# Kernel tuning notes

Hardware: AMD Instinct MI355X
Metric: run time of the kernel (lower is better)

The kernel has to match this reference:

```python
import jax, jax.numpy as jnp
import numpy as np

B, L = 32, 4096
OBS_DIM, ACT_DIM = 32, 8
D_MODEL, D_STATE, N_LAYERS = 64, 16, 2
EXPAND, D_CONV = 2, 4
D_INNER = EXPAND * D_MODEL          # 128
DT_RANK = -(-D_MODEL // 16)         # ceil(64/16) = 4


def _layer_norm(x, w, b, eps=1e-5):
    m = x.mean(-1, keepdims=True)
    v = ((x - m) ** 2).mean(-1, keepdims=True)
    return (x - m) * jax.lax.rsqrt(v + eps) * w + b


def _mamba_block(x, in_proj_W, conv_w, conv_b, x_proj_W, dt_proj_W, dt_proj_b, A_log, D, out_proj_W):
    # x: (B, L, d_model) -> (B, L, d_model)
    xz = jnp.einsum('bld,ed->ble', x, in_proj_W)              # (B, L, 2*d_inner)
    u, z = jnp.split(xz, 2, axis=-1)
    # causal depthwise conv over time (groups = d_inner)
    uc = jax.lax.conv_general_dilated(u.swapaxes(1, 2), conv_w, (1,), [(D_CONV - 1, 0)],
                                      feature_group_count=D_INNER)
    u = jax.nn.silu((uc + conv_b[None, :, None]).swapaxes(1, 2))  # (B, L, d_inner)
    proj = jnp.einsum('bld,ed->ble', u, x_proj_W)             # (B, L, dt_rank + 2*d_state)
    dt = jax.nn.softplus(jnp.einsum('blr,dr->bld', proj[..., :DT_RANK], dt_proj_W) + dt_proj_b)
    Bm = proj[..., DT_RANK:DT_RANK + D_STATE]                 # (B, L, d_state)
    Cm = proj[..., DT_RANK + D_STATE:]                        # (B, L, d_state)
    A = -jnp.exp(A_log)                                       # (d_inner, d_state)

    def step(h, inp):
        u_t, dt_t, B_t, C_t = inp                              # (B,d_inner),(B,d_inner),(B,d_state),(B,d_state)
        h = h * jnp.exp(dt_t[..., None] * A) + (dt_t * u_t)[..., None] * B_t[:, None, :]
        return h, jnp.einsum('bds,bs->bd', h, C_t)

    h0 = jnp.zeros((x.shape[0], D_INNER, D_STATE), x.dtype)
    _, ys = jax.lax.scan(step, h0, (u.swapaxes(0, 1), dt.swapaxes(0, 1),
                                    Bm.swapaxes(0, 1), Cm.swapaxes(0, 1)))
    y = ys.swapaxes(0, 1) + u * D                              # skip term D*u
    y = y * jax.nn.silu(z)                                     # gated output
    return jnp.einsum('bld,od->blo', y, out_proj_W)


def setup_inputs() -> dict:
    key = jax.random.key(0)
    ks = jax.random.split(key, 10)
    s = 0.05
    return {
        'obs': jax.random.normal(ks[0], (B, L, OBS_DIM), jnp.float32),
        'obs_mean': jnp.zeros((OBS_DIM,), jnp.float32),
        'obs_scale': jnp.ones((OBS_DIM,), jnp.float32),
        'ln_in_w': jnp.ones((OBS_DIM,), jnp.float32),
        'ln_in_b': jnp.zeros((OBS_DIM,), jnp.float32),
        'W_in': jax.random.normal(ks[1], (D_MODEL, OBS_DIM), jnp.float32) * s,
        'b_in': jnp.zeros((D_MODEL,), jnp.float32),
        'norm_w': jnp.ones((N_LAYERS, D_MODEL), jnp.float32),
        'norm_b': jnp.zeros((N_LAYERS, D_MODEL), jnp.float32),
        'in_proj_W': jax.random.normal(ks[2], (N_LAYERS, 2 * D_INNER, D_MODEL), jnp.float32) * s,
        'conv_w': jax.random.normal(ks[3], (N_LAYERS, D_INNER, 1, D_CONV), jnp.float32) * s,
        'conv_b': jnp.zeros((N_LAYERS, D_INNER), jnp.float32),
        'x_proj_W': jax.random.normal(ks[4], (N_LAYERS, DT_RANK + 2 * D_STATE, D_INNER), jnp.float32) * s,
        'dt_proj_W': jax.random.normal(ks[5], (N_LAYERS, D_INNER, DT_RANK), jnp.float32) * s,
        'dt_proj_b': jax.random.normal(ks[6], (N_LAYERS, D_INNER), jnp.float32) * s,
        'A_log': jnp.log(jnp.broadcast_to(jnp.arange(1, D_STATE + 1, dtype=jnp.float32), (N_LAYERS, D_INNER, D_STATE))),
        'D': jnp.ones((N_LAYERS, D_INNER), jnp.float32),
        'out_proj_W': jax.random.normal(ks[7], (N_LAYERS, D_MODEL, D_INNER), jnp.float32) * s,
        'W_out': jax.random.normal(ks[8], (ACT_DIM, D_MODEL), jnp.float32) * s,
        'b_out': jnp.zeros((ACT_DIM,), jnp.float32),
    }


def reference(obs, obs_mean, obs_scale, ln_in_w, ln_in_b, W_in, b_in, norm_w, norm_b,
              in_proj_W, conv_w, conv_b, x_proj_W, dt_proj_W, dt_proj_b, A_log, D,
              out_proj_W, W_out, b_out):
    x = (obs - obs_mean) / obs_scale                 # _normalize_observations
    x = _layer_norm(x, ln_in_w, ln_in_b)             # input_norm
    x = jnp.einsum('blo,do->bld', x, W_in) + b_in    # input_layer
    for i in range(N_LAYERS):                        # x = x + block(norm(x))
        x = x + _mamba_block(_layer_norm(x, norm_w[i], norm_b[i]),
                             in_proj_W[i], conv_w[i], conv_b[i], x_proj_W[i],
                             dt_proj_W[i], dt_proj_b[i], A_log[i], D[i], out_proj_W[i])
    return jnp.einsum('bld,ad->bla', x, W_out) + b_out  # output_layer
```

## Files before the change

kernel.cpp:

```cpp
#include <hip/hip_runtime.h>
#include <hip/hip_bf16.h>

#define BB 32
#define LL 4096
#define DI 128
#define DSS 16
#define NLAY 2
#define NC 128
#define CT 32
#define MROWS (BB*LL)

typedef short v8s __attribute__((ext_vector_type(8)));
typedef float v4f __attribute__((ext_vector_type(4)));
#define MFMA16(a,b,c) __builtin_amdgcn_mfma_f32_16x16x32_bf16(a,b,c,0,0,0)

#define B_X     0ull
#define B_UCOOK 16777216ull
#define B_Z     50331648ull
#define B_DTY   83886080ull
#define B_BC    117440512ull
#define B_H     125829120ull
#define B_SDT   142606336ull
#define B_WGT   144703488ull
#define B_PACK  144977920ull

#define WM_OMEAN   0
#define WM_OSCALE  32
#define WM_LNW     64
#define WM_LNB     96
#define WM_WIN     128
#define WM_BIN     2176
#define WM_NORMW   2240
#define WM_NORMB   2368
#define WM_INPROJ  2496
#define WM_CONVW   35264
#define WM_CONVB   36288
#define WM_XPROJ   36544
#define WM_DTW     45760
#define WM_DTB     46784
#define WM_ALOG    47040
#define WM_D       51136
#define WM_OUTPROJ 51392
#define WM_WOUT    67776
#define WM_BOUT    68288

#define PK_WIN 0
#define PK_INP 2048
#define PK_XP  34816
#define PK_OP  47104

__device__ __forceinline__ float ldf(const void* p, long long i, bool bf) {
  if (bf) {
    unsigned int u = ((unsigned int)((const unsigned short*)p)[i]) << 16;
    float f; __builtin_memcpy(&f, &u, 4); return f;
  }
  return ((const float*)p)[i];
}
__device__ __forceinline__ float s2f(short s){
  unsigned int u = ((unsigned int)(unsigned short)s) << 16;
  float f; __builtin_memcpy(&f, &u, 4); return f;
}
__device__ __forceinline__ short f2s(float f){
  unsigned int u; __builtin_memcpy(&u, &f, 4);
  u += 0x7fffu + ((u >> 16) & 1u);
  return (short)(u >> 16);
}
__device__ __forceinline__ float siluf(float x){
  return x * __builtin_amdgcn_rcpf(1.f + __expf(-x));
}
__device__ __forceinline__ float softplusf(float x){
  return fmaxf(x,0.f) + __logf(1.f + __expf(-fabsf(x)));
}
__device__ __forceinline__ void powtree(float e1, float pw[16]){
  pw[0]=e1; pw[1]=e1*e1; pw[3]=pw[1]*pw[1]; pw[7]=pw[3]*pw[3]; pw[15]=pw[7]*pw[7];
  pw[2]=pw[1]*e1; pw[4]=pw[3]*e1; pw[5]=pw[3]*pw[1]; pw[6]=pw[3]*pw[2];
  pw[8]=pw[7]*e1; pw[9]=pw[7]*pw[1]; pw[10]=pw[7]*pw[2]; pw[11]=pw[7]*pw[3];
  pw[12]=pw[7]*pw[4]; pw[13]=pw[7]*pw[5]; pw[14]=pw[7]*pw[6];
}

struct PtrPack { const void* p[19]; };

__global__ __launch_bounds__(256) void k_cvt(PtrPack pp, float* __restrict__ dst,
                                             short* __restrict__ pk) {
  bool bf = ((const unsigned short*)pp.p[14])[1] != 0;
  int b = blockIdx.x;
  if (b < 19) {
    const int SZ[19] = {32,32,32,32,2048,64,128,128,32768,1024,256,9216,1024,256,4096,256,16384,512,8};
    const int OF[19] = {WM_OMEAN,WM_OSCALE,WM_LNW,WM_LNB,WM_WIN,WM_BIN,WM_NORMW,WM_NORMB,
                        WM_INPROJ,WM_CONVW,WM_CONVB,WM_XPROJ,WM_DTW,WM_DTB,WM_ALOG,WM_D,
                        WM_OUTPROJ,WM_WOUT,WM_BOUT};
    const void* src = pp.p[b];
    int n = SZ[b], o = OF[b];
    for (int j = threadIdx.x; j < n; j += 256) dst[o + j] = ldf(src, j, bf);
  } else {
    int pi = b - 19;
    const int SRC[7]  = {4,8,8,11,11,16,16};
    const int LOFF[7] = {0,0,16384,0,4608,0,8192};
    const int NTA[7]  = {4,16,16,3,3,4,4};
    const int KTA[7]  = {1,2,2,4,4,4,4};
    const int KA[7]   = {32,64,64,128,128,128,128};
    const int NRA[7]  = {64,256,256,36,36,64,64};
    const int DOFF[7] = {PK_WIN, PK_INP, PK_INP+16384, PK_XP, PK_XP+6144, PK_OP, PK_OP+8192};
    const void* src = pp.p[SRC[pi]];
    int ktc = KTA[pi], K = KA[pi], nr = NRA[pi], doff = DOFF[pi], loff = LOFF[pi];
    int tot = NTA[pi]*ktc*512;
    for (int i = threadIdx.x; i < tot; i += 256) {
      int j = i & 7, lane = (i >> 3) & 63, t2 = i >> 9;
      int kt = t2 % ktc, ntile = t2 / ktc;
      int n = ntile*16 + (lane & 15);
      int k = kt*32 + (lane >> 4)*8 + j;
      float v = (n < nr) ? ldf(src, loff + (long long)n*K + k, bf) : 0.f;
      pk[doff + i] = f2s(v);
    }
  }
}

__global__ __launch_bounds__(256) void k_input(const void* __restrict__ obs,
    const float* __restrict__ wgt, const void* __restrict__ alog_raw,
    short* __restrict__ x, const short* __restrict__ pk)
{
  __shared__ short lA[64*40];
  bool bf = ((const unsigned short*)alog_raw)[1] != 0;
  int t = threadIdx.x;
  long long row0 = (long long)blockIdx.x * 64;
  {
    int m = t >> 2, q = t & 3;
    const float* om  = wgt + WM_OMEAN + q*8;
    const float* osc = wgt + WM_OSCALE + q*8;
    const float* lw  = wgt + WM_LNW + q*8;
    const float* lb  = wgt + WM_LNB + q*8;
    long long base = (row0 + m)*32 + q*8;
    float v[8]; float s1 = 0.f, s2 = 0.f;
    #pragma unroll
    for (int i = 0; i < 8; ++i) {
      float o = ldf(obs, base + i, bf);
      o = (o - om[i]) / osc[i];
      v[i] = o; s1 += o; s2 += o*o;
    }
    s1 += __shfl_xor(s1,1); s1 += __shfl_xor(s1,2);
    s2 += __shfl_xor(s2,1); s2 += __shfl_xor(s2,2);
    float mean = s1*(1.f/32.f);
    float var  = s2*(1.f/32.f) - mean*mean;
    float rs = rsqrtf(var + 1e-5f);
    #pragma unroll
    for (int i = 0; i < 8; ++i)
      lA[m*40 + q*8 + i] = f2s((v[i]-mean)*rs*lw[i] + lb[i]);
  }
  __syncthreads();
  int w = t >> 6, L = t & 63;
  v8s b = *(const v8s*)(pk + PK_WIN + (w*64 + L)*8);
  v4f zero = {0.f,0.f,0.f,0.f};
  v4f acc[4];
  #pragma unroll
  for (int mt = 0; mt < 4; ++mt) {
    v8s a = *(const v8s*)&lA[(mt*16 + (L&15))*40 + (L>>4)*8];
    acc[mt] = MFMA16(a, b, zero);
  }
  int col = w*16 + (L & 15);
  float bi = wgt[WM_BIN + col];
  #pragma unroll
  for (int mt = 0; mt < 4; ++mt)
    #pragma unroll
    for (int r = 0; r < 4; ++r) {
      int row = mt*16 + (L>>4)*4 + r;
      x[(row0+row)*64 + col] = f2s(acc[mt][r] + bi);
    }
}

__global__ __launch_bounds__(256) void k_fused1(
    const short* __restrict__ x, const float* __restrict__ wgt,
    const short* __restrict__ pk, short* __restrict__ ucook,
    short* __restrict__ z, short* __restrict__ dty,
    short* __restrict__ bcb, short* __restrict__ hbuf,
    float* __restrict__ sdtbuf, int layer)
{
  __shared__ char smem[35632];
  short* lA    = (short*)smem;
  short* lU    = (short*)smem;
  float* lnxh  = (float*)(smem + 12288);
  short* lUraw = (short*)(smem + 17408);
  float* lB    = (float*)(smem + 17408);
  float* lDtr  = (float*)(smem + 21504);
  int t = threadIdx.x;
  long long row0 = (long long)blockIdx.x * 64;
  int l0 = (int)(row0 & (LL-1));

  {
    int m = t >> 2, q = t & 3;
    const v8s* xr = (const v8s*)(x + (row0+m)*64 + q*16);
    v8s x0 = xr[0], x1 = xr[1];
    float v[16]; float s1 = 0.f, s2 = 0.f;
    #pragma unroll
    for (int j = 0; j < 8; ++j) { v[j] = s2f(x0[j]); v[8+j] = s2f(x1[j]); }
    #pragma unroll
    for (int j = 0; j < 16; ++j) { s1 += v[j]; s2 += v[j]*v[j]; }
    s1 += __shfl_xor(s1,1); s1 += __shfl_xor(s1,2);
    s2 += __shfl_xor(s2,1); s2 += __shfl_xor(s2,2);
    float mean = s1*(1.f/64.f);
    float var  = s2*(1.f/64.f) - mean*mean;
    float rs = rsqrtf(var + 1e-5f);
    const float* nw = wgt + WM_NORMW + layer*64 + q*16;
    const float* nb = wgt + WM_NORMB + layer*64 + q*16;
    #pragma unroll
    for (int j = 0; j < 16; ++j)
      lA[m*72 + q*16 + j] = f2s((v[j]-mean)*rs*nw[j] + nb[j]);
  }
  if (l0 > 0 && t < 192) {
    int hr = t >> 6, lane = t & 63;
    float xv = s2f(x[(row0 - 3 + hr)*64 + lane]);
    float s1 = xv, sq = xv*xv;
    #pragma unroll
    for (int o = 1; o < 64; o <<= 1) { s1 += __shfl_xor(s1, o); sq += __shfl_xor(sq, o); }
    float mean = s1*(1.f/64.f);
    float var  = sq*(1.f/64.f) - mean*mean;
    float rs = rsqrtf(var + 1e-5f);
    lnxh[hr*64 + lane] = (xv-mean)*rs*wgt[WM_NORMW + layer*64 + lane]
                       + wgt[WM_NORMB + layer*64 + lane];
  }
  __syncthreads();
  if (l0 > 0) {
    for (int i = t; i < 384; i += 256) {
      int hr = i >> 7, d = i & 127;
      const float* W  = wgt + WM_INPROJ + layer*16384 + d*64;
      const float* ln = lnxh + hr*64;
      float acc = 0.f;
      #pragma unroll 8
      for (int k2 = 0; k2 < 64; ++k2) acc = fmaf(ln[k2], W[k2], acc);
      lUraw[hr*136 + d] = f2s(acc);
    }
  } else {
    for (int i = t; i < 384; i += 256) lUraw[(i>>7)*136 + (i&127)] = 0;
  }
  {
    int w = t >> 6, L = t & 63;
    v8s af[4][2];
    #pragma unroll
    for (int mt = 0; mt < 4; ++mt)
      #pragma unroll
      for (int kt = 0; kt < 2; ++kt)
        af[mt][kt] = *(const v8s*)&lA[(mt*16 + (L&15))*72 + kt*32 + (L>>4)*8];
    v4f zero = {0.f,0.f,0.f,0.f};
    v4f acc[4][4];
    #pragma unroll
    for (int mt = 0; mt < 4; ++mt)
      #pragma unroll
      for (int nt = 0; nt < 4; ++nt) acc[mt][nt] = zero;
    const short* pb = pk + PK_INP + layer*16384;
    #pragma unroll
    for (int nt = 0; nt < 4; ++nt)
      #pragma unroll
      for (int kt = 0; kt < 2; ++kt) {
        v8s b = *(const v8s*)(pb + (((w*4+nt)*2 + kt)*64 + L)*8);
        #pragma unroll
        for (int mt = 0; mt < 4; ++mt)
          acc[mt][nt] = MFMA16(af[mt][kt], b, acc[mt][nt]);
      }
    #pragma unroll
    for (int nt = 0; nt < 4; ++nt) {
      int col = w*64 + nt*16 + (L & 15);
      #pragma unroll
      for (int mt = 0; mt < 4; ++mt)
        #pragma unroll
        for (int r = 0; r < 4; ++r) {
          int row = mt*16 + (L>>4)*4 + r;
          float val = acc[mt][nt][r];
          if (col < 128) lUraw[(row+3)*136 + col] = f2s(val);
          else           z[(row0+row)*DI + col-128] = f2s(val);
        }
    }
  }
  __syncthreads();
  {
    int k = t & 127, half = t >> 7, r0c = half*32;
    const float* CW = wgt + WM_CONVW + layer*512 + k*4;
    float cw0=CW[0], cw1=CW[1], cw2=CW[2], cw3=CW[3];
    float cb = wgt[WM_CONVB + layer*128 + k];
    float q0 = s2f(lUraw[(r0c+0)*136 + k]);
    float q1 = s2f(lUraw[(r0c+1)*136 + k]);
    float q2 = s2f(lUraw[(r0c+2)*136 + k]);
    #pragma unroll 4
    for (int j = 0; j < 32; ++j) {
      float q3 = s2f(lUraw[(r0c+j+3)*136 + k]);
      float cv = cb + cw0*q0 + cw1*q1 + cw2*q2 + cw3*q3;
      q0=q1; q1=q2; q2=q3;
      short cs = f2s(siluf(cv));
      lU[(r0c+j)*136 + k] = cs;
      ucook[(row0+r0c+j)*DI + k] = cs;
    }
  }
  __syncthreads();
  {
    int w = t >> 6, L = t & 63;
    v8s a[4];
    #pragma unroll
    for (int kt = 0; kt < 4; ++kt)
      a[kt] = *(const v8s*)&lU[(w*16 + (L&15))*136 + kt*32 + (L>>4)*8];
    v4f zero = {0.f,0.f,0.f,0.f};
    v4f acc[3] = {zero, zero, zero};
    const short* pb = pk + PK_XP + layer*6144;
    #pragma unroll
    for (int nt = 0; nt < 3; ++nt)
      #pragma unroll
      for (int kt = 0; kt < 4; ++kt) {
        v8s b = *(const v8s*)(pb + ((nt*4 + kt)*64 + L)*8);
        acc[nt] = MFMA16(a[kt], b, acc[nt]);
      }
    int colL = L & 15, qd = L >> 4;
    #pragma unroll
    for (int nt = 0; nt < 3; ++nt) {
      int col = nt*16 + colL;
      #pragma unroll
      for (int r = 0; r < 4; ++r) {
        int row = w*16 + qd*4 + r;
        float val = acc[nt][r];
        if (col < 4) lDtr[row*4 + col] = val;
        else if (col < 36) {
          bcb[(row0+row)*32 + col-4] = f2s(val);
          if (col < 20) lB[row*16 + col-4] = val;
        }
      }
    }
  }
  __syncthreads();
  {
    int d = t & 127, c2 = t >> 7;
    int r0s = c2*32;
    const float* AL = wgt + WM_ALOG + layer*2048 + d*16;
    float a0 = -__expf(AL[0]);
    float eps[16];
    #pragma unroll
    for (int s = 0; s < 16; ++s) eps[s] = -__expf(AL[s]) - (float)(s+1)*a0;
    const float* DWp = wgt + WM_DTW + layer*512 + d*4;
    float dw0=DWp[0], dw1=DWp[1], dw2=DWp[2], dw3=DWp[3];
    float db = wgt[WM_DTB + layer*128 + d];
    float h[16] = {};
    float sdt = 0.f;
    for (int m = 0; m < CT; ++m) {
      float4 p = *(const float4*)&lDtr[(r0s+m)*4];
      float dtv = softplusf(db + p.x*dw0 + p.y*dw1 + p.z*dw2 + p.w*dw3);
      dty[(row0+r0s+m)*DI + d] = f2s(dtv);
      float u = s2f(lU[(r0s+m)*136 + d]);
      float dtu = dtv*u; sdt += dtv;
      float e1 = __expf(dtv*a0);
      float pw[16]; powtree(e1, pw);
      float Bf[16];
      const float4* B4 = (const float4*)(lB + (r0s+m)*16);
      *(float4*)&Bf[0] = B4[0]; *(float4*)&Bf[4] = B4[1];
      *(float4*)&Bf[8] = B4[2]; *(float4*)&Bf[12] = B4[3];
      #pragma unroll
      for (int s = 0; s < 16; ++s) {
        float xx = dtv*eps[s];
        float dec = fmaf(xx, pw[s], pw[s]);
        h[s] = fmaf(h[s], dec, dtu*Bf[s]);
      }
    }
    int b = blockIdx.x >> 6;
    int c = ((blockIdx.x & 63) << 1) + c2;
    long long cidx = (long long)b*NC + c;
    #pragma unroll
    for (int s = 0; s < 16; ++s)
      hbuf[(cidx*16 + s)*DI + d] = f2s(h[s]);
    sdtbuf[cidx*DI + d] = sdt;
  }
}

__global__ __launch_bounds__(128) void k_scan2(
    short* __restrict__ hbuf, const float* __restrict__ sdtbuf,
    const float* __restrict__ wgt, int layer)
{
  int b = blockIdx.x >> 4, s = blockIdx.x & 15, d = threadIdx.x;
  float a = -__expf(wgt[WM_ALOG + layer*2048 + d*16 + s]);
  long long hstep = (long long)DSS*DI;
  long long hb = ((long long)b*NC*16 + s)*DI + d;
  long long sb = (long long)b*NC*DI + d;
  float h = 0.f;
  short hl_c = hbuf[hb];
  float sd_c = sdtbuf[sb];
  for (int c = 0; c < NC; ++c) {
    short hl_n = 0; float sd_n = 0.f;
    if (c < NC-1) {
      hl_n = hbuf[hb + (long long)(c+1)*hstep];
      sd_n = sdtbuf[sb + (long long)(c+1)*DI];
    }
    float E = __expf(a * sd_c);
    float hl = s2f(hl_c);
    hbuf[hb + (long long)c*hstep] = f2s(h);
    h = fmaf(h, E, hl);
    hl_c = hl_n; sd_c = sd_n;
  }
}

__global__ __launch_bounds__(256) void k_fused3(
    const short* __restrict__ ucook, const short* __restrict__ dty,
    const short* __restrict__ bcb, const short* __restrict__ zb,
    const short* __restrict__ hbuf, const float* __restrict__ wgt,
    const short* __restrict__ pk, short* __restrict__ x,
    const void* __restrict__ alog_raw, void* __restrict__ out,
    int layer, int do_wout)
{
  __shared__ short lY[64*136];
  __shared__ float lBC[64*32];
  int t = threadIdx.x;
  long long row0 = (long long)blockIdx.x * 64;
  for (int i = t; i < 64*32; i += 256) lBC[i] = s2f(bcb[row0*32 + i]);
  __syncthreads();
  {
    int d = t & 127, c2 = t >> 7;
    int r0s = c2*32;
    const float* AL = wgt + WM_ALOG + layer*2048 + d*16;
    float a0 = -__expf(AL[0]);
    float eps[16];
    #pragma unroll
    for (int s = 0; s < 16; ++s) eps[s] = -__expf(AL[s]) - (float)(s+1)*a0;
    float Dd = wgt[WM_D + layer*128 + d];
    int b = blockIdx.x >> 6;
    int c = ((blockIdx.x & 63) << 1) + c2;
    long long cidx = (long long)b*NC + c;
    float h[16];
    #pragma unroll
    for (int s = 0; s < 16; ++s)
      h[s] = s2f(hbuf[(cidx*16 + s)*DI + d]);
    long long rb = (row0 + r0s)*DI + d;
    short pdt = dty[rb], pu = ucook[rb], pz = zb[rb];
    for (int m = 0; m < CT; ++m) {
      short ndt = 0, nu = 0, nz = 0;
      if (m < CT-1) {
        long long rn = rb + (long long)(m+1)*DI;
        ndt = dty[rn]; nu = ucook[rn]; nz = zb[rn];
      }
      float dtv = s2f(pdt), u = s2f(pu), zv = s2f(pz);
      float dtu = dtv*u;
      float e1 = __expf(dtv*a0);
      float pw[16]; powtree(e1, pw);
      float BCf[32];
      const float4* BC4 = (const float4*)(lBC + (r0s+m)*32);
      #pragma unroll
      for (int q4 = 0; q4 < 8; ++q4) *(float4*)&BCf[q4*4] = BC4[q4];
      float y = 0.f;
      #pragma unroll
      for (int s = 0; s < 16; ++s) {
        float xx = dtv*eps[s];
        float dec = fmaf(xx, pw[s], pw[s]);
        h[s] = fmaf(h[s], dec, dtu*BCf[s]);
        y = fmaf(h[s], BCf[16+s], y);
      }
      lY[(r0s+m)*136 + d] = f2s((y + u*Dd)*siluf(zv));
      pdt = ndt; pu = nu; pz = nz;
    }
  }
  __syncthreads();
  float xnew[4][4];
  int w = t >> 6, L = t & 63;
  {
    v4f zero = {0.f,0.f,0.f,0.f};
    v4f acc[4] = {zero, zero, zero, zero};
    const short* pb = pk + PK_OP + layer*8192;
    #pragma unroll
    for (int kt = 0; kt < 4; ++kt) {
      v8s b = *(const v8s*)(pb + ((w*4 + kt)*64 + L)*8);
      #pragma unroll
      for (int mt = 0; mt < 4; ++mt) {
        v8s a = *(const v8s*)&lY[(mt*16 + (L&15))*136 + kt*32 + (L>>4)*8];
        acc[mt] = MFMA16(a, b, acc[mt]);
      }
    }
    int col = w*16 + (L & 15);
    #pragma unroll
    for (int mt = 0; mt < 4; ++mt)
      #pragma unroll
      for (int r = 0; r < 4; ++r) {
        int row = mt*16 + (L>>4)*4 + r;
        long long g = (row0+row)*64 + col;
        xnew[mt][r] = s2f(x[g]) + acc[mt][r];
        if (!do_wout) x[g] = f2s(xnew[mt][r]);
      }
  }
  if (do_wout) {
    __syncthreads();
    int col = w*16 + (L & 15);
    #pragma unroll
    for (int mt = 0; mt < 4; ++mt)
      #pragma unroll
      for (int r = 0; r < 4; ++r) {
        int row = mt*16 + (L>>4)*4 + r;
        lY[row*72 + col] = f2s(xnew[mt][r]);
      }
    __syncthreads();
    bool bf = ((const unsigned short*)alog_raw)[1] != 0;
    for (int i = t; i < 512; i += 256) {
      int m = i >> 3, aa = i & 7;
      const float* W = wgt + WM_WOUT + aa*64;
      const short* xr = &lY[m*72];
      float acc = wgt[WM_BOUT + aa];
      #pragma unroll
      for (int j8 = 0; j8 < 8; ++j8) {
        v8s xv = *(const v8s*)&xr[j8*8];
        #pragma unroll
        for (int j = 0; j < 8; ++j) acc = fmaf(s2f(xv[j]), W[j8*8+j], acc);
      }
      long long oi = (row0 + m)*8 + aa;
      if (bf) ((__hip_bfloat16*)out)[oi] = __float2bfloat16(acc);
      else    ((float*)out)[oi] = acc;
    }
  }
}

extern "C" void kernel_launch(void* const* d_in, const int* in_sizes, int n_in,
                              void* d_out, int out_size, void* d_ws, size_t ws_size,
                              hipStream_t stream)
{
  char* wsb = (char*)d_ws;
  short* x     = (short*)(wsb + B_X);
  short* ucook = (short*)(wsb + B_UCOOK);
  short* zb    = (short*)(wsb + B_Z);
  short* dty   = (short*)(wsb + B_DTY);
  short* bcb   = (short*)(wsb + B_BC);
  short* hbuf  = (short*)(wsb + B_H);
  float* sdt   = (float*)(wsb + B_SDT);
  float* wgt   = (float*)(wsb + B_WGT);
  short* pk    = (short*)(wsb + B_PACK);

  PtrPack pp;
  for (int i = 0; i < 19; ++i) pp.p[i] = d_in[i+1];
  const void* obs  = d_in[0];
  const void* alog = d_in[15];

  k_cvt  <<<dim3(26),       dim3(256), 0, stream>>>(pp, wgt, pk);
  k_input<<<dim3(MROWS/64), dim3(256), 0, stream>>>(obs, wgt, alog, x, pk);
  for (int layer = 0; layer < NLAY; ++layer) {
    k_fused1<<<dim3(MROWS/64), dim3(256), 0, stream>>>(x, wgt, pk, ucook, zb, dty, bcb,
                                                       hbuf, sdt, layer);
    k_scan2 <<<dim3(BB*DSS),   dim3(128), 0, stream>>>(hbuf, sdt, wgt, layer);
    k_fused3<<<dim3(MROWS/64), dim3(256), 0, stream>>>(ucook, dty, bcb, zb, hbuf, wgt, pk, x,
                                                       alog, d_out, layer, layer == NLAY-1);
  }
}
```

Baseline: 479.1 us.

## Split fused scan kernels into separate GEMM, scan and out-projection kernels

The fused projection+local-scan kernel and the fused scan+out-projection kernel are each split in two. The dt rank projections now go to a global float buffer, the chunk scans run in their own kernels, and the gated output is written back over ucook before a separate out-projection GEMM kernel reads it. The likely aim is to lower per-kernel LDS and register pressure so the scan phases get more occupancy, in exchange for extra global round trips and two more launches per layer. It also adds a fast path for a0 == -1 in scan1 that gets exp(dt*a0) from the softplus intermediates instead of a separate exp.

```diff
diff --git a/kernel.cpp b/kernel.cpp
--- a/kernel.cpp
+++ b/kernel.cpp
@@ -23,6 +23,7 @@
 #define B_SDT   142606336ull
 #define B_WGT   144703488ull
 #define B_PACK  144977920ull
+#define B_DTR   145104896ull
 
 #define WM_OMEAN   0
 #define WM_OSCALE  32
@@ -170,17 +171,14 @@
 __global__ __launch_bounds__(256) void k_fused1(
     const short* __restrict__ x, const float* __restrict__ wgt,
     const short* __restrict__ pk, short* __restrict__ ucook,
-    short* __restrict__ z, short* __restrict__ dty,
-    short* __restrict__ bcb, short* __restrict__ hbuf,
-    float* __restrict__ sdtbuf, int layer)
+    short* __restrict__ z, float* __restrict__ dtr,
+    short* __restrict__ bcb, int layer)
 {
   __shared__ char smem[35632];
   short* lA    = (short*)smem;
   short* lU    = (short*)smem;
   float* lnxh  = (float*)(smem + 12288);
   short* lUraw = (short*)(smem + 17408);
-  float* lB    = (float*)(smem + 17408);
-  float* lDtr  = (float*)(smem + 21504);
   int t = threadIdx.x;
   long long row0 = (long long)blockIdx.x * 64;
   int l0 = (int)(row0 & (LL-1));
@@ -313,55 +311,78 @@
       for (int r = 0; r < 4; ++r) {
         int row = w*16 + qd*4 + r;
         float val = acc[nt][r];
-        if (col < 4) lDtr[row*4 + col] = val;
-        else if (col < 36) {
-          bcb[(row0+row)*32 + col-4] = f2s(val);
-          if (col < 20) lB[row*16 + col-4] = val;
-        }
-      }
-    }
-  }
-  __syncthreads();
-  {
-    int d = t & 127, c2 = t >> 7;
-    int r0s = c2*32;
-    const float* AL = wgt + WM_ALOG + layer*2048 + d*16;
-    float a0 = -__expf(AL[0]);
-    float eps[16];
-    #pragma unroll
-    for (int s = 0; s < 16; ++s) eps[s] = -__expf(AL[s]) - (float)(s+1)*a0;
-    const float* DWp = wgt + WM_DTW + layer*512 + d*4;
-    float dw0=DWp[0], dw1=DWp[1], dw2=DWp[2], dw3=DWp[3];
-    float db = wgt[WM_DTB + layer*128 + d];
-    float h[16] = {};
-    float sdt = 0.f;
-    for (int m = 0; m < CT; ++m) {
-      float4 p = *(const float4*)&lDtr[(r0s+m)*4];
-      float dtv = softplusf(db + p.x*dw0 + p.y*dw1 + p.z*dw2 + p.w*dw3);
-      dty[(row0+r0s+m)*DI + d] = f2s(dtv);
-      float u = s2f(lU[(r0s+m)*136 + d]);
-      float dtu = dtv*u; sdt += dtv;
-      float e1 = __expf(dtv*a0);
-      float pw[16]; powtree(e1, pw);
-      float Bf[16];
-      const float4* B4 = (const float4*)(lB + (r0s+m)*16);
-      *(float4*)&Bf[0] = B4[0]; *(float4*)&Bf[4] = B4[1];
-      *(float4*)&Bf[8] = B4[2]; *(float4*)&Bf[12] = B4[3];
-      #pragma unroll
-      for (int s = 0; s < 16; ++s) {
-        float xx = dtv*eps[s];
-        float dec = fmaf(xx, pw[s], pw[s]);
-        h[s] = fmaf(h[s], dec, dtu*Bf[s]);
-      }
-    }
-    int b = blockIdx.x >> 6;
-    int c = ((blockIdx.x & 63) << 1) + c2;
-    long long cidx = (long long)b*NC + c;
-    #pragma unroll
-    for (int s = 0; s < 16; ++s)
-      hbuf[(cidx*16 + s)*DI + d] = f2s(h[s]);
-    sdtbuf[cidx*DI + d] = sdt;
-  }
+        if (col < 4)       dtr[(row0+row)*4 + col] = val;
+        else if (col < 36) bcb[(row0+row)*32 + col-4] = f2s(val);
+      }
+    }
+  }
+}
+
+__global__ __launch_bounds__(256) void k_scan1(
+    const short* __restrict__ ucook, const float* __restrict__ dtr,
+    const short* __restrict__ bcb, const float* __restrict__ wgt,
+    short* __restrict__ dty, short* __restrict__ hbuf,
+    float* __restrict__ sdtbuf, int layer)
+{
+  __shared__ float lB[64*16];
+  __shared__ float lDtr[64*4];
+  int t = threadIdx.x;
+  long long row0 = (long long)blockIdx.x * 64;
+  for (int i = t; i < 64*16; i += 256) {
+    int m = i >> 4, s = i & 15;
+    lB[i] = s2f(bcb[(row0+m)*32 + s]);
+  }
+  if (t < 256) lDtr[t] = dtr[row0*4 + t];
+  __syncthreads();
+  int d = t & 127, c2 = t >> 7;
+  int r0s = c2*32;
+  const float* AL = wgt + WM_ALOG + layer*2048 + d*16;
+  float a0 = -__expf(AL[0]);
+  bool a0one = (a0 == -1.0f);
+  float eps[16];
+  #pragma unroll
+  for (int s = 0; s < 16; ++s) eps[s] = -__expf(AL[s]) - (float)(s+1)*a0;
+  const float* DWp = wgt + WM_DTW + layer*512 + d*4;
+  float dw0=DWp[0], dw1=DWp[1], dw2=DWp[2], dw3=DWp[3];
+  float db = wgt[WM_DTB + layer*128 + d];
+  float h[16] = {};
+  float sdt = 0.f;
+  for (int m = 0; m < CT; ++m) {
+    long long row = row0 + r0s + m;
+    float4 p = *(const float4*)&lDtr[(r0s+m)*4];
+    float v = db + p.x*dw0 + p.y*dw1 + p.z*dw2 + p.w*dw3;
+    float dtv, e1;
+    if (a0one) {
+      float te = __expf(-fabsf(v));
+      float r  = __builtin_amdgcn_rcpf(1.f + te);
+      e1  = (v > 0.f) ? te*r : r;
+      dtv = fmaxf(v, 0.f) - __logf(r);
+    } else {
+      dtv = softplusf(v);
+      e1  = __expf(dtv*a0);
+    }
+    dty[row*DI + d] = f2s(dtv);
+    float u = s2f(ucook[row*DI + d]);
+    float dtu = dtv*u; sdt += dtv;
+    float pw[16]; powtree(e1, pw);
+    float Bf[16];
+    const float4* B4 = (const float4*)(lB + (r0s+m)*16);
+    *(float4*)&Bf[0] = B4[0]; *(float4*)&Bf[4] = B4[1];
+    *(float4*)&Bf[8] = B4[2]; *(float4*)&Bf[12] = B4[3];
+    #pragma unroll
+    for (int s = 0; s < 16; ++s) {
+      float xx = dtv*eps[s];
+      float dec = fmaf(xx, pw[s], pw[s]);
+      h[s] = fmaf(h[s], dec, dtu*Bf[s]);
+    }
+  }
+  int b = blockIdx.x >> 6;
+  int c = ((blockIdx.x & 63) << 1) + c2;
+  long long cidx = (long long)b*NC + c;
+  #pragma unroll
+  for (int s = 0; s < 16; ++s)
+    hbuf[(cidx*16 + s)*DI + d] = f2s(h[s]);
+  sdtbuf[cidx*DI + d] = sdt;
 }
 
 __global__ __launch_bounds__(128) void k_scan2(
@@ -390,63 +411,79 @@
   }
 }
 
-__global__ __launch_bounds__(256) void k_fused3(
-    const short* __restrict__ ucook, const short* __restrict__ dty,
+__global__ __launch_bounds__(256) void k_scan3(
+    short* __restrict__ ucook, const short* __restrict__ dty,
     const short* __restrict__ bcb, const short* __restrict__ zb,
     const short* __restrict__ hbuf, const float* __restrict__ wgt,
-    const short* __restrict__ pk, short* __restrict__ x,
-    const void* __restrict__ alog_raw, void* __restrict__ out,
-    int layer, int do_wout)
-{
-  __shared__ short lY[64*136];
+    int layer)
+{
   __shared__ float lBC[64*32];
   int t = threadIdx.x;
   long long row0 = (long long)blockIdx.x * 64;
   for (int i = t; i < 64*32; i += 256) lBC[i] = s2f(bcb[row0*32 + i]);
   __syncthreads();
-  {
-    int d = t & 127, c2 = t >> 7;
-    int r0s = c2*32;
-    const float* AL = wgt + WM_ALOG + layer*2048 + d*16;
-    float a0 = -__expf(AL[0]);
-    float eps[16];
-    #pragma unroll
-    for (int s = 0; s < 16; ++s) eps[s] = -__expf(AL[s]) - (float)(s+1)*a0;
-    float Dd = wgt[WM_D + layer*128 + d];
-    int b = blockIdx.x >> 6;
-    int c = ((blockIdx.x & 63) << 1) + c2;
-    long long cidx = (long long)b*NC + c;
-    float h[16];
-    #pragma unroll
-    for (int s = 0; s < 16; ++s)
-      h[s] = s2f(hbuf[(cidx*16 + s)*DI + d]);
-    long long rb = (row0 + r0s)*DI + d;
-    short pdt = dty[rb], pu = ucook[rb], pz = zb[rb];
-    for (int m = 0; m < CT; ++m) {
-      short ndt = 0, nu = 0, nz = 0;
-      if (m < CT-1) {
-        long long rn = rb + (long long)(m+1)*DI;
-        ndt = dty[rn]; nu = ucook[rn]; nz = zb[rn];
-      }
-      float dtv = s2f(pdt), u = s2f(pu), zv = s2f(pz);
-      float dtu = dtv*u;
-      float e1 = __expf(dtv*a0);
-      float pw[16]; powtree(e1, pw);
-      float BCf[32];
-      const float4* BC4 = (const float4*)(lBC + (r0s+m)*32);
-      #pragma unroll
-      for (int q4 = 0; q4 < 8; ++q4) *(float4*)&BCf[q4*4] = BC4[q4];
-      float y = 0.f;
-      #pragma unroll
-      for (int s = 0; s < 16; ++s) {
-        float xx = dtv*eps[s];
-        float dec = fmaf(xx, pw[s], pw[s]);
-        h[s] = fmaf(h[s], dec, dtu*BCf[s]);
-        y = fmaf(h[s], BCf[16+s], y);
-      }
-      lY[(r0s+m)*136 + d] = f2s((y + u*Dd)*siluf(zv));
-      pdt = ndt; pu = nu; pz = nz;
-    }
+  int d = t & 127, c2 = t >> 7;
+  int r0s = c2*32;
+  const float* AL = wgt + WM_ALOG + layer*2048 + d*16;
+  float a0 = -__expf(AL[0]);
+  float eps[16];
+  #pragma unroll
+  for (int s = 0; s < 16; ++s) eps[s] = -__expf(AL[s]) - (float)(s+1)*a0;
+  float Dd = wgt[WM_D + layer*128 + d];
+  int b = blockIdx.x >> 6;
+  int c = ((blockIdx.x & 63) << 1) + c2;
+  long long cidx = (long long)b*NC + c;
+  float h[16];
+  #pragma unroll
+  for (int s = 0; s < 16; ++s)
+    h[s] = s2f(hbuf[(cidx*16 + s)*DI + d]);
+  long long rb = (row0 + r0s)*DI + d;
+  short pdt = dty[rb], pu = ucook[rb], pz = zb[rb];
+  for (int m = 0; m < CT; ++m) {
+    short ndt = 0, nu = 0, nz = 0;
+    if (m < CT-1) {
+      long long rn = rb + (long long)(m+1)*DI;
+      ndt = dty[rn]; nu = ucook[rn]; nz = zb[rn];
+    }
+    float dtv = s2f(pdt), u = s2f(pu), zv = s2f(pz);
+    float dtu = dtv*u;
+    float e1 = __expf(dtv*a0);
+    float pw[16]; powtree(e1, pw);
+    float BCf[32];
+    const float4* BC4 = (const float4*)(lBC + (r0s+m)*32);
+    #pragma unroll
+    for (int q4 = 0; q4 < 8; ++q4) *(float4*)&BCf[q4*4] = BC4[q4];
+    float y = 0.f;
+    #pragma unroll
+    for (int s = 0; s < 16; ++s) {
+      float xx = dtv*eps[s];
+      float dec = fmaf(xx, pw[s], pw[s]);
+      h[s] = fmaf(h[s], dec, dtu*BCf[s]);
+      y = fmaf(h[s], BCf[16+s], y);
+    }
+    ucook[rb + (long long)m*DI] = f2s((y + u*Dd)*siluf(zv));
+    pdt = ndt; pu = nu; pz = nz;
+  }
+}
+
+__global__ __launch_bounds__(256) void k_outproj(
+    const short* __restrict__ yg, const float* __restrict__ wgt,
+    const short* __restrict__ pk, short* __restrict__ x,
+    const void* __restrict__ alog_raw, void* __restrict__ out,
+    int layer, int do_wout)
+{
+  __shared__ short lY[64*136];
+  int t = threadIdx.x;
+  long long row0 = (long long)blockIdx.x * 64;
+  {
+    int m = t >> 2, q = t & 3;
+    const v8s* src = (const v8s*)(yg + (row0+m)*DI + q*32);
+    v8s v0 = src[0], v1 = src[1], v2 = src[2], v3 = src[3];
+    short* dstp = &lY[m*136 + q*32];
+    *(v8s*)(dstp+0)  = v0;
+    *(v8s*)(dstp+8)  = v1;
+    *(v8s*)(dstp+16) = v2;
+    *(v8s*)(dstp+24) = v3;
   }
   __syncthreads();
   float xnew[4][4];
@@ -519,6 +556,7 @@
   float* sdt   = (float*)(wsb + B_SDT);
   float* wgt   = (float*)(wsb + B_WGT);
   short* pk    = (short*)(wsb + B_PACK);
+  float* dtr   = (float*)(wsb + B_DTR);
 
   PtrPack pp;
   for (int i = 0; i < 19; ++i) pp.p[i] = d_in[i+1];
@@ -528,10 +566,11 @@
   k_cvt  <<<dim3(26),       dim3(256), 0, stream>>>(pp, wgt, pk);
   k_input<<<dim3(MROWS/64), dim3(256), 0, stream>>>(obs, wgt, alog, x, pk);
   for (int layer = 0; layer < NLAY; ++layer) {
-    k_fused1<<<dim3(MROWS/64), dim3(256), 0, stream>>>(x, wgt, pk, ucook, zb, dty, bcb,
-                                                       hbuf, sdt, layer);
-    k_scan2 <<<dim3(BB*DSS),   dim3(128), 0, stream>>>(hbuf, sdt, wgt, layer);
-    k_fused3<<<dim3(MROWS/64), dim3(256), 0, stream>>>(ucook, dty, bcb, zb, hbuf, wgt, pk, x,
-                                                       alog, d_out, layer, layer == NLAY-1);
-  }
-}
+    k_fused1 <<<dim3(MROWS/64), dim3(256), 0, stream>>>(x, wgt, pk, ucook, zb, dtr, bcb, layer);
+    k_scan1  <<<dim3(MROWS/64), dim3(256), 0, stream>>>(ucook, dtr, bcb, wgt, dty, hbuf, sdt, layer);
+    k_scan2  <<<dim3(BB*DSS),   dim3(128), 0, stream>>>(hbuf, sdt, wgt, layer);
+    k_scan3  <<<dim3(MROWS/64), dim3(256), 0, stream>>>(ucook, dty, bcb, zb, hbuf, wgt, layer);
+    k_outproj<<<dim3(MROWS/64), dim3(256), 0, stream>>>(ucook, wgt, pk, x, alog, d_out,
+                                                        layer, layer == NLAY-1);
+  }
+}
```

New measurement: 544.8 us. 13.7% more time.

## Shrink fused1 LDS footprint, specialize softplus/exp for unit A, vectorize BC load

Applied to the files above, without the earlier changes.

Rearranges shared memory in the first fused kernel so the conv output is written back in place over the raw buffer. A temporary holds the three overlapping rows across a barrier, which cuts LDS per block and may raise occupancy. When A_log[0] gives a0 == -1, one exp serves both softplus and exp(dt*a0), using the identity exp(-softplus(v)) = sigmoid(-v). The BC staging loop in fused3 becomes a single 8-wide vector load per thread. The in-place reuse adds an extra barrier and depends on careful row ordering to avoid races.

```diff
diff --git a/kernel.cpp b/kernel.cpp
--- a/kernel.cpp
+++ b/kernel.cpp
@@ -174,13 +174,12 @@
     short* __restrict__ bcb, short* __restrict__ hbuf,
     float* __restrict__ sdtbuf, int layer)
 {
-  __shared__ char smem[35632];
+  __shared__ char smem[28208];
   short* lA    = (short*)smem;
-  short* lU    = (short*)smem;
-  float* lnxh  = (float*)(smem + 12288);
-  short* lUraw = (short*)(smem + 17408);
-  float* lB    = (float*)(smem + 17408);
-  float* lDtr  = (float*)(smem + 21504);
+  float* lB    = (float*)smem;
+  float* lDtr  = (float*)(smem + 4096);
+  float* lnxh  = (float*)(smem + 9216);
+  short* lUraw = (short*)(smem + 9984);
   int t = threadIdx.x;
   long long row0 = (long long)blockIdx.x * 64;
   int l0 = (int)(row0 & (LL-1));
@@ -278,14 +277,31 @@
     float q0 = s2f(lUraw[(r0c+0)*136 + k]);
     float q1 = s2f(lUraw[(r0c+1)*136 + k]);
     float q2 = s2f(lUraw[(r0c+2)*136 + k]);
-    #pragma unroll 4
-    for (int j = 0; j < 32; ++j) {
+    short b0 = 0, b1 = 0, b2 = 0;
+    #pragma unroll
+    for (int j = 0; j < 3; ++j) {
       float q3 = s2f(lUraw[(r0c+j+3)*136 + k]);
       float cv = cb + cw0*q0 + cw1*q1 + cw2*q2 + cw3*q3;
       q0=q1; q1=q2; q2=q3;
       short cs = f2s(siluf(cv));
-      lU[(r0c+j)*136 + k] = cs;
       ucook[(row0+r0c+j)*DI + k] = cs;
+      if (half == 0) lUraw[(r0c+j)*136 + k] = cs;
+      else { if (j==0) b0=cs; else if (j==1) b1=cs; else b2=cs; }
+    }
+    #pragma unroll 4
+    for (int j = 3; j < 32; ++j) {
+      float q3 = s2f(lUraw[(r0c+j+3)*136 + k]);
+      float cv = cb + cw0*q0 + cw1*q1 + cw2*q2 + cw3*q3;
+      q0=q1; q1=q2; q2=q3;
+      short cs = f2s(siluf(cv));
+      ucook[(row0+r0c+j)*DI + k] = cs;
+      lUraw[(r0c+j)*136 + k] = cs;
+    }
+    __syncthreads();
+    if (half == 1) {
+      lUraw[32*136 + k] = b0;
+      lUraw[33*136 + k] = b1;
+      lUraw[34*136 + k] = b2;
     }
   }
   __syncthreads();
@@ -294,7 +310,7 @@
     v8s a[4];
     #pragma unroll
     for (int kt = 0; kt < 4; ++kt)
-      a[kt] = *(const v8s*)&lU[(w*16 + (L&15))*136 + kt*32 + (L>>4)*8];
+      a[kt] = *(const v8s*)&lUraw[(w*16 + (L&15))*136 + kt*32 + (L>>4)*8];
     v4f zero = {0.f,0.f,0.f,0.f};
     v4f acc[3] = {zero, zero, zero};
     const short* pb = pk + PK_XP + layer*6144;
@@ -327,6 +343,7 @@
     int r0s = c2*32;
     const float* AL = wgt + WM_ALOG + layer*2048 + d*16;
     float a0 = -__expf(AL[0]);
+    bool a0one = (a0 == -1.0f);
     float eps[16];
     #pragma unroll
     for (int s = 0; s < 16; ++s) eps[s] = -__expf(AL[s]) - (float)(s+1)*a0;
@@ -336,12 +353,22 @@
     float h[16] = {};
     float sdt = 0.f;
     for (int m = 0; m < CT; ++m) {
+      long long row = row0 + r0s + m;
       float4 p = *(const float4*)&lDtr[(r0s+m)*4];
-      float dtv = softplusf(db + p.x*dw0 + p.y*dw1 + p.z*dw2 + p.w*dw3);
-      dty[(row0+r0s+m)*DI + d] = f2s(dtv);
-      float u = s2f(lU[(r0s+m)*136 + d]);
+      float v = db + p.x*dw0 + p.y*dw1 + p.z*dw2 + p.w*dw3;
+      float dtv, e1;
+      if (a0one) {
+        float te = __expf(-fabsf(v));
+        float r  = __builtin_amdgcn_rcpf(1.f + te);
+        e1  = (v > 0.f) ? te*r : r;
+        dtv = fmaxf(v, 0.f) - __logf(r);
+      } else {
+        dtv = softplusf(v);
+        e1  = __expf(dtv*a0);
+      }
+      dty[row*DI + d] = f2s(dtv);
+      float u = s2f(lUraw[(r0s+m)*136 + d]);
       float dtu = dtv*u; sdt += dtv;
-      float e1 = __expf(dtv*a0);
       float pw[16]; powtree(e1, pw);
       float Bf[16];
       const float4* B4 = (const float4*)(lB + (r0s+m)*16);
@@ -402,7 +429,12 @@
   __shared__ float lBC[64*32];
   int t = threadIdx.x;
   long long row0 = (long long)blockIdx.x * 64;
-  for (int i = t; i < 64*32; i += 256) lBC[i] = s2f(bcb[row0*32 + i]);
+  {
+    v8s v = *(const v8s*)(bcb + row0*32 + t*8);
+    float* dst = lBC + t*8;
+    #pragma unroll
+    for (int j = 0; j < 8; ++j) dst[j] = s2f(v[j]);
+  }
   __syncthreads();
   {
     int d = t & 127, c2 = t >> 7;
```

New measurement: 485.7 us. Within noise of the previous version (+1.4%).
